# Optimization experiments

Hardware: AMD Instinct MI355X
Metric: run time of the kernel (lower is better)

The kernel has to match this reference:

```python
import jax, jax.numpy as jnp
import numpy as np

EMBED_DIM = 1024
RANK = 32

def setup_inputs() -> dict:
    key = jax.random.key(0)
    ks = jax.random.split(key, 9)
    B, S, D, R = 4, 4096, EMBED_DIM, RANK
    s_in = 1.0 / np.sqrt(D)
    s_r = 1.0 / np.sqrt(R)
    return {
        "x": jax.random.normal(ks[0], (B, S, D), dtype=jnp.float32),
        # Linear weights stored as [in, out] (transpose of torch layout)
        "Wq": jax.random.uniform(ks[1], (D, R), jnp.float32, -s_in, s_in),
        "bq": jax.random.uniform(ks[2], (R,), jnp.float32, -s_in, s_in),
        "Wk": jax.random.uniform(ks[3], (D, R), jnp.float32, -s_in, s_in),
        "bk": jax.random.uniform(ks[4], (R,), jnp.float32, -s_in, s_in),
        "Wv": jax.random.uniform(ks[5], (D, R), jnp.float32, -s_in, s_in),
        "bv": jax.random.uniform(ks[6], (R,), jnp.float32, -s_in, s_in),
        "Wo": jax.random.uniform(ks[7], (R, D), jnp.float32, -s_r, s_r),
        "bo": jax.random.uniform(ks[8], (D,), jnp.float32, -s_r, s_r),
    }

def reference(x, Wq, bq, Wk, bk, Wv, bv, Wo, bo):
    scale = RANK ** (-0.5)
    Q = jnp.einsum('bsd,dr->bsr', x, Wq) + bq  # [B,S,R]
    K = jnp.einsum('bsd,dr->bsr', x, Wk) + bk
    V = jnp.einsum('bsd,dr->bsr', x, Wv) + bv
    scores = jnp.einsum('bqr,bkr->bqk', Q, K) * scale  # [B,S,S]
    probs = jax.nn.softmax(scores, axis=-1)
    # dropout is identity in eval mode
    attn_out = jnp.einsum('bqk,bkr->bqr', probs, V)  # [B,S,R]
    return jnp.einsum('bsr,rd->bsd', attn_out, Wo) + bo
```

## Files before the change

kernel.cpp:

```cpp
#include <hip/hip_runtime.h>

typedef __bf16 bf16x8 __attribute__((ext_vector_type(8)));
typedef float f32x4 __attribute__((ext_vector_type(4)));

#define MFMA16(a, b, c) __builtin_amdgcn_mfma_f32_16x16x32_bf16((a), (b), (c), 0, 0, 0)

#define WT_OFF   0
#define WOT_OFF  98304
#define QB_OFF   131072
#define KB_OFF   655360
#define VT_OFF   1179648

#define SCALE_QL (0.17677669529663689f * 1.4426950408889634f)

__device__ __forceinline__ void load_lds16(void* lds, const void* gsrc) {
  __builtin_amdgcn_global_load_lds(
      (const __attribute__((address_space(1))) unsigned int*)gsrc,
      (__attribute__((address_space(3))) unsigned int*)lds, 16, 0, 0);
}

__global__ __launch_bounds__(256) void prep_kernel(
    const float* __restrict__ Wq, const float* __restrict__ Wk,
    const float* __restrict__ Wv, const float* __restrict__ Wo,
    __bf16* __restrict__ ws) {
  int idx = blockIdx.x * 256 + threadIdx.x;
  if (idx < 98304) {
    int n = idx >> 10, d = idx & 1023;
    float v;
    if (n < 32)      v = Wq[d * 32 + n] * SCALE_QL;
    else if (n < 64) v = Wk[d * 32 + (n - 32)];
    else             v = Wv[d * 32 + (n - 64)];
    ws[WT_OFF + idx] = (__bf16)v;
  } else if (idx < 131072) {
    int j = idx - 98304;
    int d = j >> 5, r = j & 31;
    ws[WOT_OFF + j] = (__bf16)Wo[r * 1024 + d];
  }
}

__device__ __forceinline__ void stage_x(float* lbase, const float* x, int r0,
                                        int tt, int lane) {
#pragma unroll
  for (int j = 0; j < 4; ++j) {
    int row = j * 4 + (lane >> 4);
    int ch = lane & 15;
    int gc = (ch & 8) | ((ch & 7) ^ (row & 7));
    const float* src = x + (size_t)(r0 + row) * 1024 + tt * 64 + gc * 4;
    load_lds16(lbase + j * 256, src);
  }
}

__device__ __forceinline__ void load_w(bf16x8* w, const __bf16* Wt, int t,
                                       int c, int g) {
#pragma unroll
  for (int ks = 0; ks < 2; ++ks)
#pragma unroll
    for (int nf = 0; nf < 6; ++nf)
      w[ks * 6 + nf] =
          *(const bf16x8*)(Wt + (size_t)(nf * 16 + c) * 1024 + t * 64 + ks * 32 + g * 8);
}

__global__ __launch_bounds__(64) void proj_kernel(
    const float* __restrict__ x, const float* __restrict__ bq,
    const float* __restrict__ bk, const float* __restrict__ bv,
    __bf16* __restrict__ ws) {
  __shared__ float xlds[4 * 16 * 64];
  const __bf16* Wt = ws + WT_OFF;
  __bf16* Qb = ws + QB_OFF;
  __bf16* Kb = ws + KB_OFF;
  __bf16* Vt = ws + VT_OFF;
  int lane = threadIdx.x;
  int c = lane & 15, g = lane >> 4;
  int r0 = blockIdx.x * 16;

#pragma unroll
  for (int tt = 0; tt < 4; ++tt) stage_x(xlds + tt * 1024, x, r0, tt, lane);
  __builtin_amdgcn_sched_barrier(0);
  bf16x8 wcur[12], wnext[12];
  load_w(wcur, Wt, 0, c, g);
  __builtin_amdgcn_sched_barrier(0);

  f32x4 acc[6];
#pragma unroll
  for (int i = 0; i < 6; ++i) acc[i] = (f32x4){0.f, 0.f, 0.f, 0.f};

  for (int t = 0; t < 16; ++t) {
    __builtin_amdgcn_sched_barrier(0);
    if (t + 1 < 16) load_w(wnext, Wt, t + 1, c, g);
    __builtin_amdgcn_sched_barrier(0);
    if (t == 0)      asm volatile("s_waitcnt vmcnt(12)" ::: "memory");
    else if (t < 12) asm volatile("s_waitcnt vmcnt(16)" ::: "memory");
    else             asm volatile("s_waitcnt vmcnt(0)" ::: "memory");
    __builtin_amdgcn_sched_barrier(0);

    const float* xt = xlds + (t & 3) * 1024;
#pragma unroll
    for (int ks = 0; ks < 2; ++ks) {
      int cha = (ks << 3) | ((2 * g) ^ (c & 7));
      int chb = (ks << 3) | (((2 * g) | 1) ^ (c & 7));
      f32x4 xa = *(const f32x4*)(xt + c * 64 + cha * 4);
      f32x4 xb = *(const f32x4*)(xt + c * 64 + chb * 4);
      bf16x8 a;
      a[0] = (__bf16)xa[0]; a[1] = (__bf16)xa[1];
      a[2] = (__bf16)xa[2]; a[3] = (__bf16)xa[3];
      a[4] = (__bf16)xb[0]; a[5] = (__bf16)xb[1];
      a[6] = (__bf16)xb[2]; a[7] = (__bf16)xb[3];
#pragma unroll
      for (int nf = 0; nf < 6; ++nf)
        acc[nf] = MFMA16(a, wcur[ks * 6 + nf], acc[nf]);
    }
    __builtin_amdgcn_sched_barrier(0);
    if (t + 4 < 16) stage_x(xlds + (t & 3) * 1024, x, r0, t + 4, lane);
#pragma unroll
    for (int i = 0; i < 12; ++i) wcur[i] = wnext[i];
  }

#pragma unroll
  for (int nf = 0; nf < 6; ++nf) {
    int n = nf * 16 + c;
    float bias = (n < 32) ? bq[n] * SCALE_QL : (n < 64 ? bk[n - 32] : bv[n - 64]);
#pragma unroll
    for (int r = 0; r < 4; ++r) {
      int row = r0 + 4 * g + r;
      float v = acc[nf][r] + bias;
      if (n < 32)      Qb[row * 32 + n] = (__bf16)v;
      else if (n < 64) Kb[row * 32 + (n - 32)] = (__bf16)v;
      else {
        int batch = row >> 12, s = row & 4095;
        Vt[((size_t)(batch * 32 + (n - 64))) * 4096 + s] = (__bf16)v;
      }
    }
  }
}

__device__ __forceinline__ void stage_kv(__bf16* buf, const __bf16* Kbb,
                                         const __bf16* Vtb, int kt, int w,
                                         int lane) {
  if (w < 2) {
#pragma unroll
    for (int i = 0; i < 2; ++i) {
      int row = w * 32 + i * 16 + (lane >> 2);
      int ch = lane & 3;
      const __bf16* src = Kbb + (size_t)(kt * 64 + row) * 32 + ch * 8;
      load_lds16(buf + w * 1024 + i * 512, src);
    }
  } else {
    int t2 = w - 2;
#pragma unroll
    for (int i = 0; i < 2; ++i) {
      int row = t2 * 16 + i * 8 + (lane >> 3);
      int ch = lane & 7;
      int gc = ch ^ (row & 7);
      const __bf16* src = Vtb + (size_t)row * 4096 + kt * 64 + gc * 8;
      load_lds16(buf + 2048 + t2 * 1024 + i * 512, src);
    }
  }
}

__global__ __launch_bounds__(256) void flash_kernel(
    const float* __restrict__ bo, float* __restrict__ out,
    const __bf16* __restrict__ ws) {
  const __bf16* Wot = ws + WOT_OFF;
  const __bf16* Qb  = ws + QB_OFF;
  const __bf16* Kb  = ws + KB_OFF;
  const __bf16* Vt  = ws + VT_OFF;
  __shared__ __bf16 kv[2][4096];
  __shared__ __bf16 pbuf[4][16 * 72];
  __shared__ __bf16 abuf[4][16 * 40];
  int tid = threadIdx.x;
  int w = tid >> 6, lane = tid & 63, c = lane & 15, g = lane >> 4;
  int batch = blockIdx.x >> 6, qb = blockIdx.x & 63;
  int qrow0 = batch * 4096 + qb * 64 + w * 16;
  const __bf16* Kbb = Kb + (size_t)batch * 4096 * 32;
  const __bf16* Vtb = Vt + (size_t)batch * 32 * 4096;

  const f32x4 zero = {0.f, 0.f, 0.f, 0.f};
  bf16x8 qfrag = *(const bf16x8*)(Qb + (size_t)(qrow0 + c) * 32 + g * 8);
  f32x4 acc0 = zero, acc1 = zero;
  float m = -1e30f, lsum = 0.f;

  stage_kv(kv[0], Kbb, Vtb, 0, w, lane);

  for (int kt = 0; kt < 64; ++kt) {
    __syncthreads();
    if (kt + 1 < 64) stage_kv(kv[(kt + 1) & 1], Kbb, Vtb, kt + 1, w, lane);
    const __bf16* kvb = kv[kt & 1];

    bf16x8 ak[4], av[4];
#pragma unroll
    for (int i = 0; i < 4; ++i)
      ak[i] = *(const bf16x8*)(kvb + (i * 16 + c) * 32 + g * 8);
#pragma unroll
    for (int t2 = 0; t2 < 2; ++t2)
#pragma unroll
      for (int ks = 0; ks < 2; ++ks)
        av[t2 * 2 + ks] = *(const bf16x8*)(kvb + 2048 + (t2 * 16 + c) * 64 +
                                           (((ks << 2) | g) ^ (c & 7)) * 8);

    f32x4 sr[4];
#pragma unroll
    for (int i = 0; i < 4; ++i) sr[i] = MFMA16(ak[i], qfrag, zero);

    float mx = sr[0][0];
#pragma unroll
    for (int i = 0; i < 4; ++i)
#pragma unroll
      for (int r = 0; r < 4; ++r) mx = fmaxf(mx, sr[i][r]);
    mx = fmaxf(mx, __shfl_xor(mx, 16, 64));
    mx = fmaxf(mx, __shfl_xor(mx, 32, 64));
    float mn = fmaxf(m, mx);
    float corr = exp2f(m - mn);
    m = mn;
    float ps = 0.f;
    float p[4][4];
#pragma unroll
    for (int i = 0; i < 4; ++i)
#pragma unroll
      for (int r = 0; r < 4; ++r) {
        p[i][r] = exp2f(sr[i][r] - mn);
        ps += p[i][r];
      }
    ps += __shfl_xor(ps, 16, 64);
    ps += __shfl_xor(ps, 32, 64);
    lsum = lsum * corr + ps;
#pragma unroll
    for (int r = 0; r < 4; ++r) { acc0[r] *= corr; acc1[r] *= corr; }

    __bf16* pw = pbuf[w] + c * 72;
#pragma unroll
    for (int i = 0; i < 4; ++i)
#pragma unroll
      for (int r = 0; r < 4; ++r)
        pw[16 * i + 4 * g + r] = (__bf16)p[i][r];
    asm volatile("s_waitcnt lgkmcnt(0)" ::: "memory");
    __builtin_amdgcn_sched_barrier(0);
    bf16x8 pf0 = *(const bf16x8*)(pbuf[w] + c * 72 + g * 8);
    bf16x8 pf1 = *(const bf16x8*)(pbuf[w] + c * 72 + 32 + g * 8);

    acc0 = MFMA16(av[0], pf0, acc0);
    acc0 = MFMA16(av[1], pf1, acc0);
    acc1 = MFMA16(av[2], pf0, acc1);
    acc1 = MFMA16(av[3], pf1, acc1);
  }

  float inv = 1.0f / lsum;
#pragma unroll
  for (int r = 0; r < 4; ++r) { acc0[r] *= inv; acc1[r] *= inv; }
  __bf16* aw = abuf[w] + c * 40;
#pragma unroll
  for (int r = 0; r < 4; ++r) {
    aw[4 * g + r] = (__bf16)acc0[r];
    aw[16 + 4 * g + r] = (__bf16)acc1[r];
  }
  asm volatile("s_waitcnt lgkmcnt(0)" ::: "memory");
  __builtin_amdgcn_sched_barrier(0);
  bf16x8 aa = *(const bf16x8*)(abuf[w] + c * 40 + g * 8);
#pragma unroll 4
  for (int nf = 0; nf < 64; ++nf) {
    bf16x8 bw = *(const bf16x8*)(Wot + (nf * 16 + c) * 32 + g * 8);
    f32x4 o = MFMA16(aa, bw, zero);
    float bias = bo[nf * 16 + c];
    float* op = out + (size_t)(qrow0 + 4 * g) * 1024 + nf * 16 + c;
#pragma unroll
    for (int r = 0; r < 4; ++r) op[(size_t)r * 1024] = o[r] + bias;
  }
}

extern "C" void kernel_launch(void* const* d_in, const int* in_sizes, int n_in,
                              void* d_out, int out_size, void* d_ws, size_t ws_size,
                              hipStream_t stream) {
  const float* x  = (const float*)d_in[0];
  const float* Wq = (const float*)d_in[1];
  const float* bq = (const float*)d_in[2];
  const float* Wk = (const float*)d_in[3];
  const float* bk = (const float*)d_in[4];
  const float* Wv = (const float*)d_in[5];
  const float* bv = (const float*)d_in[6];
  const float* Wo = (const float*)d_in[7];
  const float* bo = (const float*)d_in[8];
  float* out = (float*)d_out;
  __bf16* ws = (__bf16*)d_ws;
  prep_kernel<<<dim3(512), dim3(256), 0, stream>>>(Wq, Wk, Wv, Wo, ws);
  proj_kernel<<<dim3(1024), dim3(64), 0, stream>>>(x, bq, bk, bv, ws);
  flash_kernel<<<dim3(256), dim3(256), 0, stream>>>(bo, out, ws);
}
```

Measured before the change: 218.4 us.

## Split KV sequence across waves with in-block softmax merge, quadruple grid

The flash kernel changes from 64 query rows per block (one 16-row tile per wave) to 16 query rows per block, with the four waves each handling a quarter of the key sequence. Partial accumulators and (max, sum) pairs are merged through shared memory, and each wave then computes a quarter of the output projection columns. The grid grows from 256 to 1024 blocks to fill more CUs, LDS staging of K/V is replaced by direct global loads, and the P conversion uses packed bf16 conversion instructions. In exchange, the K/V tiles are no longer shared across four query tiles through LDS, so global/L2 traffic for K and V increases fourfold.

```diff
diff --git a/kernel.cpp b/kernel.cpp
--- a/kernel.cpp
+++ b/kernel.cpp
@@ -2,6 +2,7 @@
 
 typedef __bf16 bf16x8 __attribute__((ext_vector_type(8)));
 typedef float f32x4 __attribute__((ext_vector_type(4)));
+typedef unsigned int u32;
 
 #define MFMA16(a, b, c) __builtin_amdgcn_mfma_f32_16x16x32_bf16((a), (b), (c), 0, 0, 0)
 
@@ -133,69 +134,42 @@
   }
 }
 
-__device__ __forceinline__ void stage_kv(__bf16* buf, const __bf16* Kbb,
-                                         const __bf16* Vtb, int kt, int w,
-                                         int lane) {
-  if (w < 2) {
-#pragma unroll
-    for (int i = 0; i < 2; ++i) {
-      int row = w * 32 + i * 16 + (lane >> 2);
-      int ch = lane & 3;
-      const __bf16* src = Kbb + (size_t)(kt * 64 + row) * 32 + ch * 8;
-      load_lds16(buf + w * 1024 + i * 512, src);
-    }
-  } else {
-    int t2 = w - 2;
-#pragma unroll
-    for (int i = 0; i < 2; ++i) {
-      int row = t2 * 16 + i * 8 + (lane >> 3);
-      int ch = lane & 7;
-      int gc = ch ^ (row & 7);
-      const __bf16* src = Vtb + (size_t)row * 4096 + kt * 64 + gc * 8;
-      load_lds16(buf + 2048 + t2 * 1024 + i * 512, src);
-    }
-  }
-}
-
-__global__ __launch_bounds__(256) void flash_kernel(
+__global__ __launch_bounds__(256, 4) void flash_kernel(
     const float* __restrict__ bo, float* __restrict__ out,
     const __bf16* __restrict__ ws) {
   const __bf16* Wot = ws + WOT_OFF;
   const __bf16* Qb  = ws + QB_OFF;
   const __bf16* Kb  = ws + KB_OFF;
   const __bf16* Vt  = ws + VT_OFF;
-  __shared__ __bf16 kv[2][4096];
   __shared__ __bf16 pbuf[4][16 * 72];
-  __shared__ __bf16 abuf[4][16 * 40];
+  __shared__ float  pacc[4][32 * 16];
+  __shared__ float2 mlbuf[4][16];
+  __shared__ __bf16 abuf[16 * 40];
   int tid = threadIdx.x;
   int w = tid >> 6, lane = tid & 63, c = lane & 15, g = lane >> 4;
-  int batch = blockIdx.x >> 6, qb = blockIdx.x & 63;
-  int qrow0 = batch * 4096 + qb * 64 + w * 16;
+  int batch = blockIdx.x >> 8, qt = blockIdx.x & 255;
+  int qrow0 = batch * 4096 + qt * 16;
   const __bf16* Kbb = Kb + (size_t)batch * 4096 * 32;
   const __bf16* Vtb = Vt + (size_t)batch * 32 * 4096;
+  int kbase = w * 1024;
 
   const f32x4 zero = {0.f, 0.f, 0.f, 0.f};
   bf16x8 qfrag = *(const bf16x8*)(Qb + (size_t)(qrow0 + c) * 32 + g * 8);
   f32x4 acc0 = zero, acc1 = zero;
   float m = -1e30f, lsum = 0.f;
 
-  stage_kv(kv[0], Kbb, Vtb, 0, w, lane);
-
-  for (int kt = 0; kt < 64; ++kt) {
-    __syncthreads();
-    if (kt + 1 < 64) stage_kv(kv[(kt + 1) & 1], Kbb, Vtb, kt + 1, w, lane);
-    const __bf16* kvb = kv[kt & 1];
-
+  for (int kt = 0; kt < 16; ++kt) {
+    int k0 = kbase + kt * 64;
     bf16x8 ak[4], av[4];
 #pragma unroll
     for (int i = 0; i < 4; ++i)
-      ak[i] = *(const bf16x8*)(kvb + (i * 16 + c) * 32 + g * 8);
+      ak[i] = *(const bf16x8*)(Kbb + (size_t)(k0 + i * 16 + c) * 32 + g * 8);
 #pragma unroll
     for (int t2 = 0; t2 < 2; ++t2)
 #pragma unroll
       for (int ks = 0; ks < 2; ++ks)
-        av[t2 * 2 + ks] = *(const bf16x8*)(kvb + 2048 + (t2 * 16 + c) * 64 +
-                                           (((ks << 2) | g) ^ (c & 7)) * 8);
+        av[t2 * 2 + ks] =
+            *(const bf16x8*)(Vtb + (size_t)(t2 * 16 + c) * 4096 + k0 + ks * 32 + g * 8);
 
     f32x4 sr[4];
 #pragma unroll
@@ -211,27 +185,26 @@
     float mn = fmaxf(m, mx);
     float corr = exp2f(m - mn);
     m = mn;
+
     float ps = 0.f;
-    float p[4][4];
-#pragma unroll
-    for (int i = 0; i < 4; ++i)
-#pragma unroll
-      for (int r = 0; r < 4; ++r) {
-        p[i][r] = exp2f(sr[i][r] - mn);
-        ps += p[i][r];
-      }
+    __bf16* pw = pbuf[w] + c * 72;
+#pragma unroll
+    for (int i = 0; i < 4; ++i) {
+      float p0 = exp2f(sr[i][0] - mn), p1 = exp2f(sr[i][1] - mn);
+      float p2 = exp2f(sr[i][2] - mn), p3 = exp2f(sr[i][3] - mn);
+      ps += (p0 + p1) + (p2 + p3);
+      u32 lo, hi;
+      asm("v_cvt_pk_bf16_f32 %0, %1, %2" : "=v"(lo) : "v"(p0), "v"(p1));
+      asm("v_cvt_pk_bf16_f32 %0, %1, %2" : "=v"(hi) : "v"(p2), "v"(p3));
+      uint2 pr; pr.x = lo; pr.y = hi;
+      *(uint2*)(pw + 16 * i + 4 * g) = pr;
+    }
     ps += __shfl_xor(ps, 16, 64);
     ps += __shfl_xor(ps, 32, 64);
     lsum = lsum * corr + ps;
 #pragma unroll
     for (int r = 0; r < 4; ++r) { acc0[r] *= corr; acc1[r] *= corr; }
 
-    __bf16* pw = pbuf[w] + c * 72;
-#pragma unroll
-    for (int i = 0; i < 4; ++i)
-#pragma unroll
-      for (int r = 0; r < 4; ++r)
-        pw[16 * i + 4 * g + r] = (__bf16)p[i][r];
     asm volatile("s_waitcnt lgkmcnt(0)" ::: "memory");
     __builtin_amdgcn_sched_barrier(0);
     bf16x8 pf0 = *(const bf16x8*)(pbuf[w] + c * 72 + g * 8);
@@ -243,21 +216,38 @@
     acc1 = MFMA16(av[3], pf1, acc1);
   }
 
-  float inv = 1.0f / lsum;
-#pragma unroll
-  for (int r = 0; r < 4; ++r) { acc0[r] *= inv; acc1[r] *= inv; }
-  __bf16* aw = abuf[w] + c * 40;
 #pragma unroll
   for (int r = 0; r < 4; ++r) {
-    aw[4 * g + r] = (__bf16)acc0[r];
-    aw[16 + 4 * g + r] = (__bf16)acc1[r];
-  }
-  asm volatile("s_waitcnt lgkmcnt(0)" ::: "memory");
-  __builtin_amdgcn_sched_barrier(0);
-  bf16x8 aa = *(const bf16x8*)(abuf[w] + c * 40 + g * 8);
+    pacc[w][(4 * g + r) * 16 + c] = acc0[r];
+    pacc[w][(16 + 4 * g + r) * 16 + c] = acc1[r];
+  }
+  if (g == 0) { float2 ml; ml.x = m; ml.y = lsum; mlbuf[w][c] = ml; }
+  __syncthreads();
+
+#pragma unroll
+  for (int p2 = 0; p2 < 2; ++p2) {
+    int idx = tid + p2 * 256;
+    int q = idx & 15, rv = idx >> 4;
+    float M = mlbuf[0][q].x;
+#pragma unroll
+    for (int w2 = 1; w2 < 4; ++w2) M = fmaxf(M, mlbuf[w2][q].x);
+    float L = 0.f, val = 0.f;
+#pragma unroll
+    for (int w2 = 0; w2 < 4; ++w2) {
+      float2 ml = mlbuf[w2][q];
+      float sc = exp2f(ml.x - M);
+      L += ml.y * sc;
+      val += pacc[w2][rv * 16 + q] * sc;
+    }
+    abuf[q * 40 + rv] = (__bf16)(val / L);
+  }
+  __syncthreads();
+
+  bf16x8 aa = *(const bf16x8*)(abuf + c * 40 + g * 8);
 #pragma unroll 4
-  for (int nf = 0; nf < 64; ++nf) {
-    bf16x8 bw = *(const bf16x8*)(Wot + (nf * 16 + c) * 32 + g * 8);
+  for (int j = 0; j < 16; ++j) {
+    int nf = w * 16 + j;
+    bf16x8 bw = *(const bf16x8*)(Wot + (size_t)(nf * 16 + c) * 32 + g * 8);
     f32x4 o = MFMA16(aa, bw, zero);
     float bias = bo[nf * 16 + c];
     float* op = out + (size_t)(qrow0 + 4 * g) * 1024 + nf * 16 + c;
@@ -282,5 +272,5 @@
   __bf16* ws = (__bf16*)d_ws;
   prep_kernel<<<dim3(512), dim3(256), 0, stream>>>(Wq, Wk, Wv, Wo, ws);
   proj_kernel<<<dim3(1024), dim3(64), 0, stream>>>(x, bq, bk, bv, ws);
-  flash_kernel<<<dim3(256), dim3(256), 0, stream>>>(bo, out, ws);
-}
+  flash_kernel<<<dim3(1024), dim3(256), 0, stream>>>(bo, out, ws);
+}
```

Result: faster. 193.6 us (-11.4%).
